# Performance work log

Measured on AMD Instinct MI355X. Metric: run time of the kernel, lower is better.

## Reference

```python
import jax, jax.numpy as jnp
import numpy as np

N_NODES = 50000
N_EDGES = 400000
H, D = 4, 32  # num_heads, per-head dim
NEG_SLOPE = 0.1


def setup_inputs() -> dict:
    key = jax.random.key(0)
    ks = jax.random.split(key, 12)
    inp = {
        'features': jax.random.normal(ks[0], (N_NODES, 256), jnp.float32) * 0.1,
        'src': jax.random.randint(ks[1], (N_EDGES,), 0, N_NODES, jnp.int32),
        'dst': jax.random.randint(ks[2], (N_EDGES,), 0, N_NODES, jnp.int32),
        'w': jax.random.uniform(ks[3], (N_EDGES,), jnp.float32),
        'W1': jax.random.normal(ks[4], (256, 128), jnp.float32) * 0.05,
        'al1': jax.random.normal(ks[5], (H, D), jnp.float32) * 0.1,
        'ar1': jax.random.normal(ks[6], (H, D), jnp.float32) * 0.1,
        'W2': jax.random.normal(ks[7], (128, 128), jnp.float32) * 0.05,
        'al2': jax.random.normal(ks[8], (H, D), jnp.float32) * 0.1,
        'ar2': jax.random.normal(ks[9], (H, D), jnp.float32) * 0.1,
        'Wout': jax.random.normal(ks[10], (256, 128), jnp.float32) * 0.05,
        'bout': jnp.zeros((128,), jnp.float32),
    }
    return inp


def _gat_layer(x, W, al, ar, src, dst, w):
    # x: [N, in_dim] -> ft: [N, H, D]
    ft = (x @ W).reshape(-1, H, D)
    el = jnp.einsum('nhd,hd->nh', ft, al)  # left attention logits per node
    er = jnp.einsum('nhd,hd->nh', ft, ar)
    # edge logits: leaky_relu(el[src] + er[dst]), then edge-weight scaling
    e = jax.nn.leaky_relu(el[src] + er[dst], negative_slope=NEG_SLOPE)  # [E, H]
    e = w[:, None] * e
    # segment softmax over incoming edges of each destination node
    m = jax.ops.segment_max(e, dst, num_segments=N_NODES)  # [N, H]
    a = jnp.exp(e - m[dst])
    s = jax.ops.segment_sum(a, dst, num_segments=N_NODES)
    a = a / s[dst]  # [E, H]
    # weighted scatter-sum aggregation: rst[dst] += a * ft[src]
    msg = ft[src] * a[:, :, None]  # [E, H, D]
    rst = jax.ops.segment_sum(msg, dst, num_segments=N_NODES)  # [N, H, D]
    # activation=relu, then concat heads (contiguous -> reshape)
    return jax.nn.relu(rst).reshape(-1, H * D)


def reference(features, src, dst, w, W1, al1, ar1, W2, al2, ar2, Wout, bout):
    x1 = _gat_layer(features, W1, al1, ar1, src, dst, w)  # [N, 128]
    x2 = _gat_layer(x1, W2, al2, ar2, src, dst, w)        # [N, 128]
    h = jnp.concatenate([x1, x2], axis=-1)                # [N, 256]
    return h @ Wout + bout                                # [N, 128]
```

## Files before the change

### kernel.cpp

```cpp
#include <hip/hip_runtime.h>
#include <math.h>

#define NEG_SLOPE 0.1f

typedef unsigned short u16;
typedef unsigned int u32;
typedef _Float16 f16;
typedef f16 f16x2 __attribute__((ext_vector_type(2)));
typedef f16 f16x8 __attribute__((ext_vector_type(8)));
typedef float f32x4 __attribute__((ext_vector_type(4)));

#define GLLDS16(g, l) __builtin_amdgcn_global_load_lds( \
    (const __attribute__((address_space(1))) void*)(g), \
    (__attribute__((address_space(3))) void*)(l), 16, 0, 0)


__device__ __forceinline__ void cast_panel(const float* __restrict__ W,
                                           const float* __restrict__ al,
                                           const float* __restrict__ ar,
                                           u16* __restrict__ bp, int t, int NC) {
    int per_kt = NC * 16;
    int kt = t / per_kt;
    int rem = t - kt * per_kt;
    int nt = rem >> 8;
    int w32 = rem & 255;
    int kg = w32 >> 6;
    int col = (w32 >> 2) & 15;
    int kp = (w32 & 3) * 2;
    int n = nt * 16 + col;
    int k = kt * 32 + kg * 8 + kp;
    float v0 = 0.f, v1 = 0.f;
    if (n < 128) {
        v0 = W[(size_t)k * 128 + n];
        v1 = W[(size_t)(k + 1) * 128 + n];
    } else if (n < 136) {
        const float* av = (n < 132) ? al : ar;
        int h = (n < 132) ? (n - 128) : (n - 132);
        float s0 = 0.f, s1 = 0.f;
        for (int d = 0; d < 32; d++) {
            float a = av[h * 32 + d];
            s0 += W[(size_t)k * 128 + h * 32 + d] * a;
            s1 += W[(size_t)(k + 1) * 128 + h * 32 + d] * a;
        }
        v0 = s0; v1 = s1;
    }
    f16x2 p;
    p.x = (f16)v0; p.y = (f16)v1;
    *(f16x2*)&((u32*)bp)[t] = p;
}

__global__ void histcast_k(const int* __restrict__ dst, int* __restrict__ cnt, int E,
                           const float* __restrict__ W1, const float* __restrict__ al1,
                           const float* __restrict__ ar1, u16* __restrict__ b1,
                           const float* __restrict__ W2, const float* __restrict__ al2,
                           const float* __restrict__ ar2, u16* __restrict__ b2,
                           const float* __restrict__ W3, u16* __restrict__ b3) {
    int t = blockIdx.x * 256 + threadIdx.x;
    if (t < E) atomicAdd(&cnt[dst[t]], 1);
    if (t < 18432) cast_panel(W1, al1, ar1, b1, t, 144);
    else if (t < 27648) cast_panel(W2, al2, ar2, b2, t - 18432, 144);
    else if (t < 44032) cast_panel(W3, nullptr, nullptr, b3, t - 27648, 128);
}


__global__ void assign_k(const int* __restrict__ cnt, int* __restrict__ start,
                         int* __restrict__ ctr, int N) {
    __shared__ int s[256];
    __shared__ int base;
    int t = threadIdx.x;
    int i = blockIdx.x * 256 + t;
    int v = (i < N) ? cnt[i] : 0;
    s[t] = v;
    __syncthreads();
    int incl = v;
    for (int off = 1; off < 256; off <<= 1) {
        int add = (t >= off) ? s[t - off] : 0;
        __syncthreads();
        incl += add;
        s[t] = incl;
        __syncthreads();
    }
    if (t == 255) base = atomicAdd(ctr, incl);
    __syncthreads();
    if (i < N) start[i] = base + incl - v;
}


template <int NT>
__device__ __forceinline__ void gemm_tile(
        const void* __restrict__ Av, int a_is_f16, int lda,
        const u16* __restrict__ Bp,
        const float* __restrict__ bias, float* __restrict__ Cf,
        u16* __restrict__ Ch, float* __restrict__ el, float* __restrict__ er,
        int M, int K, int tile, char* shmem) {
    u16* As = (u16*)shmem;
    u16* Bs = (u16*)(shmem + 8192);
    int tid = threadIdx.x;
    int wv = tid >> 6, lane = tid & 63;
    int mrow = lane & 15;
    int row0 = tile * 64;

    f32x4 acc[NT];
#pragma unroll
    for (int nt = 0; nt < NT; nt++) acc[nt] = (f32x4){0.f, 0.f, 0.f, 0.f};

    for (int k0 = 0; k0 < K; k0 += 64) {
        int kt0 = k0 >> 5;
        const u16* Bsrc = Bp + (size_t)kt0 * (NT * 512);
#pragma unroll
        for (int i = 0; i < (2 * NT * 64 + 255) / 256; i++) {
            int c = tid + i * 256;
            if (c < 2 * NT * 64) GLLDS16(Bsrc + (size_t)c * 8, &Bs[c * 8]);
        }
#pragma unroll
        for (int i = 0; i < 2; i++) {
            int c = tid + i * 256;
            int slice = c >> 8, w32 = c & 255;
            int rblk = w32 >> 6, kg = (w32 >> 4) & 3, rr = w32 & 15;
            int row = row0 + rblk * 16 + rr;
            int k = k0 + slice * 32 + kg * 8;
            if (a_is_f16) {
                const u16* Ah = (const u16*)Av;
                GLLDS16(Ah + (size_t)row * lda + k, &As[c * 8]);
            } else {
                const float* Af = (const float*)Av;
                if (row > M - 1) row = M - 1;
                const float* ap = &Af[(size_t)row * lda + k];
                float4 v0 = *(const float4*)ap;
                float4 v1 = *(const float4*)(ap + 4);
                f16x8 pk;
                pk[0] = (f16)v0.x; pk[1] = (f16)v0.y; pk[2] = (f16)v0.z; pk[3] = (f16)v0.w;
                pk[4] = (f16)v1.x; pk[5] = (f16)v1.y; pk[6] = (f16)v1.z; pk[7] = (f16)v1.w;
                *(f16x8*)&As[c * 8] = pk;
            }
        }
        __syncthreads();
#pragma unroll
        for (int kk = 0; kk < 2; kk++) {
            f16x8 ah = *(const f16x8*)&As[kk * 2048 + wv * 512 + lane * 8];
#pragma unroll
            for (int nt = 0; nt < NT; nt++) {
                f16x8 bh = *(const f16x8*)&Bs[kk * (NT * 512) + nt * 512 + lane * 8];
                acc[nt] = __builtin_amdgcn_mfma_f32_16x16x32_f16(ah, bh, acc[nt], 0, 0, 0);
            }
        }
        __syncthreads();
    }

    int rbase = row0 + wv * 16 + (lane >> 4) * 4;
#pragma unroll
    for (int nt = 0; nt < 8; nt++) {
        int col = nt * 16 + mrow;
        float bv = bias ? bias[col] : 0.f;
        f32x4 v = acc[nt];
#pragma unroll
        for (int reg = 0; reg < 4; reg++) {
            int rr = rbase + reg;
            if (rr < M) {
                float val = v[reg] + bv;
                if (Cf) Cf[(size_t)rr * 128 + col] = val;
                if (Ch) *(f16*)&Ch[(size_t)rr * 128 + col] = (f16)val;
            }
        }
    }
    if (NT == 9) {
        f32x4 v = acc[8];
#pragma unroll
        for (int reg = 0; reg < 4; reg++) {
            int rr = rbase + reg;
            if (rr < M) {
                if (mrow < 4) el[rr * 4 + mrow] = v[reg];
                else if (mrow < 8) er[rr * 4 + (mrow - 4)] = v[reg];
            }
        }
    }
}

template <int NT>
__global__ __launch_bounds__(256) void gemm_k(
        const void* __restrict__ Av, int a_is_f16, int lda,
        const u16* __restrict__ Bp, const float* __restrict__ bias,
        float* __restrict__ Cf, u16* __restrict__ Ch,
        float* __restrict__ el, float* __restrict__ er, int M, int K) {
    alignas(16) __shared__ char sh[8192 + NT * 2048];
    gemm_tile<NT>(Av, a_is_f16, lda, Bp, bias, Cf, Ch, el, er, M, K, blockIdx.x, sh);
}

__global__ __launch_bounds__(256) void g1s_k(
        const float* __restrict__ features, const u16* __restrict__ b1,
        u16* __restrict__ fth, float* __restrict__ el, float* __restrict__ er,
        int M, int gb,
        const int* __restrict__ src, const int* __restrict__ dst,
        const float* __restrict__ w, const int* __restrict__ start,
        int* __restrict__ fill, int2* __restrict__ edge_s, int E) {
    alignas(16) __shared__ char sh[8192 + 9 * 2048];
    if ((int)blockIdx.x < gb) {
        gemm_tile<9>(features, 0, 256, b1, nullptr, nullptr, fth, el, er,
                     M, 256, blockIdx.x, sh);
    } else {
        int e = (blockIdx.x - gb) * 256 + threadIdx.x;
        if (e < E) {
            int d = dst[e];
            int pos = atomicAdd(&fill[d], 1);
            edge_s[start[d] + pos] = make_int2(src[e], __float_as_int(w[e]));
        }
    }
}


__device__ __forceinline__ float lrelu(float x) {
    return x > 0.f ? x : NEG_SLOPE * x;
}

__global__ __launch_bounds__(256) void agg_k(const u32* __restrict__ fth2,
                                             const float4* __restrict__ el4,
                                             const float4* __restrict__ er4,
                                             const int2* __restrict__ edge_s,
                                             const int* __restrict__ start,
                                             const int* __restrict__ cnt,
                                             u16* __restrict__ xcat,
                                             int ooff, int N, int ngroups) {
    __shared__ float4 sA[256];
    __shared__ int sS[256];
    int wv = threadIdx.x >> 6;
    int lane = threadIdx.x & 63;
    int head = lane >> 4;
    for (int g = blockIdx.x; g < ngroups; g += gridDim.x) {
        int n = g * 4 + wv;
        if (n >= N) continue;
        int r0 = start[n], deg = cnt[n];
        u16* op = &xcat[(size_t)n * 256 + ooff + 2 * lane];
        if (deg == 0) {
            *(u32*)op = 0;
            continue;
        }
        float4 ern = er4[n];
        float acc0 = 0.f, acc1 = 0.f;
        if (deg <= 64) {
            float4 a = make_float4(0.f, 0.f, 0.f, 0.f);
            int s = 0;
            if (lane < deg) {
                int2 ep = edge_s[r0 + lane];
                s = ep.x;
                float we = __int_as_float(ep.y);
                float4 e = el4[s];
                a.x = __expf(we * lrelu(e.x + ern.x));
                a.y = __expf(we * lrelu(e.y + ern.y));
                a.z = __expf(we * lrelu(e.z + ern.z));
                a.w = __expf(we * lrelu(e.w + ern.w));
            }
            float4 sm = a;
            for (int m = 1; m < deg; m <<= 1) {
                sm.x += __shfl_xor(sm.x, m);
                sm.y += __shfl_xor(sm.y, m);
                sm.z += __shfl_xor(sm.z, m);
                sm.w += __shfl_xor(sm.w, m);
            }
            a.x *= __builtin_amdgcn_rcpf(sm.x);
            a.y *= __builtin_amdgcn_rcpf(sm.y);
            a.z *= __builtin_amdgcn_rcpf(sm.z);
            a.w *= __builtin_amdgcn_rcpf(sm.w);
            sA[wv * 64 + lane] = a;
            sS[wv * 64 + lane] = s;
            const float* sAf = (const float*)&sA[wv * 64];
            const int* sSp = &sS[wv * 64];
            int i = 0;
            for (; i + 8 <= deg; i += 8) {
                float wg[8];
                u32 pp[8];
#pragma unroll
                for (int j = 0; j < 8; j++) {
                    wg[j] = sAf[(i + j) * 4 + head];
                    pp[j] = fth2[(size_t)sSp[i + j] * 64 + lane];
                }
#pragma unroll
                for (int j = 0; j < 8; j++) {
                    f16x2 hp = *(const f16x2*)&pp[j];
                    acc0 += wg[j] * (float)hp.x;
                    acc1 += wg[j] * (float)hp.y;
                }
            }
            for (; i < deg; i++) {
                float wgt = sAf[i * 4 + head];
                u32 p = fth2[(size_t)sSp[i] * 64 + lane];
                f16x2 hp = *(const f16x2*)&p;
                acc0 += wgt * (float)hp.x;
                acc1 += wgt * (float)hp.y;
            }
        } else {
            float4 mx = make_float4(-INFINITY, -INFINITY, -INFINITY, -INFINITY);
            for (int i = lane; i < deg; i += 64) {
                int2 ep = edge_s[r0 + i];
                float we = __int_as_float(ep.y);
                float4 e = el4[ep.x];
                mx.x = fmaxf(mx.x, we * lrelu(e.x + ern.x));
                mx.y = fmaxf(mx.y, we * lrelu(e.y + ern.y));
                mx.z = fmaxf(mx.z, we * lrelu(e.z + ern.z));
                mx.w = fmaxf(mx.w, we * lrelu(e.w + ern.w));
            }
            for (int m = 32; m >= 1; m >>= 1) {
                mx.x = fmaxf(mx.x, __shfl_xor(mx.x, m));
                mx.y = fmaxf(mx.y, __shfl_xor(mx.y, m));
                mx.z = fmaxf(mx.z, __shfl_xor(mx.z, m));
                mx.w = fmaxf(mx.w, __shfl_xor(mx.w, m));
            }
            float4 sm = make_float4(0.f, 0.f, 0.f, 0.f);
            for (int i = lane; i < deg; i += 64) {
                int2 ep = edge_s[r0 + i];
                float we = __int_as_float(ep.y);
                float4 e = el4[ep.x];
                sm.x += __expf(we * lrelu(e.x + ern.x) - mx.x);
                sm.y += __expf(we * lrelu(e.y + ern.y) - mx.y);
                sm.z += __expf(we * lrelu(e.z + ern.z) - mx.z);
                sm.w += __expf(we * lrelu(e.w + ern.w) - mx.w);
            }
            for (int m = 32; m >= 1; m >>= 1) {
                sm.x += __shfl_xor(sm.x, m);
                sm.y += __shfl_xor(sm.y, m);
                sm.z += __shfl_xor(sm.z, m);
                sm.w += __shfl_xor(sm.w, m);
            }
            float4 inv;
            inv.x = 1.f / sm.x; inv.y = 1.f / sm.y;
            inv.z = 1.f / sm.z; inv.w = 1.f / sm.w;
            for (int i = 0; i < deg; i++) {
                int2 ep = edge_s[r0 + i];
                int si = ep.x;
                float we = __int_as_float(ep.y);
                float4 e = el4[si];
                float ax = __expf(we * lrelu(e.x + ern.x) - mx.x) * inv.x;
                float ay = __expf(we * lrelu(e.y + ern.y) - mx.y) * inv.y;
                float az = __expf(we * lrelu(e.z + ern.z) - mx.z) * inv.z;
                float aw = __expf(we * lrelu(e.w + ern.w) - mx.w) * inv.w;
                float wgt = head == 0 ? ax : (head == 1 ? ay : (head == 2 ? az : aw));
                u32 p = fth2[(size_t)si * 64 + lane];
                f16x2 hp = *(const f16x2*)&p;
                acc0 += wgt * (float)hp.x;
                acc1 += wgt * (float)hp.y;
            }
        }
        f16x2 hv;
        hv.x = (f16)fmaxf(acc0, 0.f);
        hv.y = (f16)fmaxf(acc1, 0.f);
        *(f16x2*)op = hv;
    }
}


extern "C" void kernel_launch(void* const* d_in, const int* in_sizes, int n_in,
                              void* d_out, int out_size, void* d_ws, size_t ws_size,
                              hipStream_t stream) {
    const float* features = (const float*)d_in[0];
    const int* src = (const int*)d_in[1];
    const int* dst = (const int*)d_in[2];
    const float* w = (const float*)d_in[3];
    const float* W1 = (const float*)d_in[4];
    const float* al1 = (const float*)d_in[5];
    const float* ar1 = (const float*)d_in[6];
    const float* W2 = (const float*)d_in[7];
    const float* al2 = (const float*)d_in[8];
    const float* ar2 = (const float*)d_in[9];
    const float* Wout = (const float*)d_in[10];
    const float* bout = (const float*)d_in[11];
    float* out = (float*)d_out;

    int N = in_sizes[0] / 256;
    int E = in_sizes[1];
    int Mpad = ((N + 127) / 128) * 128;

    char* ws = (char*)d_ws;
    size_t off = 0;
    auto alloc = [&](size_t bytes) -> void* {
        void* p = ws + off;
        off = (off + bytes + 255) & ~(size_t)255;
        return p;
    };
    size_t Nr = ((size_t)N * 4 + 255) & ~(size_t)255;
    int* cnt = (int*)alloc(2 * Nr + 256);
    int* fill = (int*)((char*)cnt + Nr);
    int* ctr = (int*)((char*)cnt + 2 * Nr);
    int* start = (int*)alloc((size_t)N * 4);
    int2* edge_s = (int2*)alloc((size_t)E * 8);
    u16* fth = (u16*)alloc((size_t)Mpad * 128 * 2);
    float* el = (float*)alloc((size_t)N * 4 * 4);
    float* er = (float*)alloc((size_t)N * 4 * 4);
    u16* xcat = (u16*)alloc((size_t)Mpad * 256 * 2);
    u16* b1 = (u16*)alloc((size_t)18432 * 4);
    u16* b2 = (u16*)alloc((size_t)9216 * 4);
    u16* b3 = (u16*)alloc((size_t)16384 * 4);
    (void)ws_size; (void)n_in; (void)out_size;

    (void)hipMemsetAsync(cnt, 0, 2 * Nr + 256, stream);

    int eb = (E + 255) / 256;
    int nb = (N + 255) / 256;
    int ng = (N + 3) / 4;
    int ab = ng < 2048 ? ng : 2048;
    int gb = Mpad / 64;

    histcast_k<<<eb, 256, 0, stream>>>(dst, cnt, E, W1, al1, ar1, b1,
                                       W2, al2, ar2, b2, Wout, b3);
    assign_k<<<nb, 256, 0, stream>>>(cnt, start, ctr, N);

    g1s_k<<<gb + eb, 256, 0, stream>>>(features, b1, fth, el, er, N, gb,
                                       src, dst, w, start, fill, edge_s, E);
    agg_k<<<ab, 256, 0, stream>>>((const u32*)fth, (const float4*)el, (const float4*)er,
                                  edge_s, start, cnt, xcat, 0, N, ng);

    gemm_k<9><<<gb, 256, 0, stream>>>(xcat, 1, 256, b2, nullptr,
                                      nullptr, fth, el, er, N, 128);
    agg_k<<<ab, 256, 0, stream>>>((const u32*)fth, (const float4*)el, (const float4*)er,
                                  edge_s, start, cnt, xcat, 128, N, ng);

    gemm_k<8><<<gb, 256, 0, stream>>>(xcat, 1, 256, b3, bout,
                                      out, nullptr, nullptr, nullptr, N, 256);
}
```

Before: 247.6 us.

## Fuse neighbor aggregation with following GEMM into single aggemm kernel

Replaces separate agg_k and gemm_k launches with a fused aggemm_k kernel. Each block aggregates 64 destination rows directly into the LDS A-tile in MFMA layout, then runs the GEMM from shared memory. Layer-1 output is still written to global memory for reuse as half of the final concat input. Feature buffers are double-buffered to avoid read/write hazards. This removes two launches and the global round trip of aggregated features. The cost is less parallelism: only gb blocks each do 16 sequential nodes per wave, where the old agg kernel used up to 2048 blocks with a grid-stride loop.

New measurement: 329.4 us. 33.0% more time.

```diff
diff --git a/kernel.cpp b/kernel.cpp
--- a/kernel.cpp
+++ b/kernel.cpp
@@ -176,16 +176,6 @@
     }
 }
 
-template <int NT>
-__global__ __launch_bounds__(256) void gemm_k(
-        const void* __restrict__ Av, int a_is_f16, int lda,
-        const u16* __restrict__ Bp, const float* __restrict__ bias,
-        float* __restrict__ Cf, u16* __restrict__ Ch,
-        float* __restrict__ el, float* __restrict__ er, int M, int K) {
-    alignas(16) __shared__ char sh[8192 + NT * 2048];
-    gemm_tile<NT>(Av, a_is_f16, lda, Bp, bias, Cf, Ch, el, er, M, K, blockIdx.x, sh);
-}
-
 __global__ __launch_bounds__(256) void g1s_k(
         const float* __restrict__ features, const u16* __restrict__ b1,
         u16* __restrict__ fth, float* __restrict__ el, float* __restrict__ er,
@@ -212,137 +202,229 @@
     return x > 0.f ? x : NEG_SLOPE * x;
 }
 
-__global__ __launch_bounds__(256) void agg_k(const u32* __restrict__ fth2,
-                                             const float4* __restrict__ el4,
-                                             const float4* __restrict__ er4,
-                                             const int2* __restrict__ edge_s,
-                                             const int* __restrict__ start,
-                                             const int* __restrict__ cnt,
-                                             u16* __restrict__ xcat,
-                                             int ooff, int N, int ngroups) {
-    __shared__ float4 sA[256];
+__device__ __forceinline__ u32 agg_node(const u32* __restrict__ fth2,
+                                        const float4* __restrict__ el4,
+                                        const float4* __restrict__ er4,
+                                        const int2* __restrict__ edge_s,
+                                        const int* __restrict__ start,
+                                        const int* __restrict__ cnt,
+                                        int n, int lane, int head,
+                                        float4* sAw, int* sSw) {
+    int r0 = start[n], deg = cnt[n];
+    if (deg == 0) return 0u;
+    float4 ern = er4[n];
+    float acc0 = 0.f, acc1 = 0.f;
+    if (deg <= 64) {
+        float4 a = make_float4(0.f, 0.f, 0.f, 0.f);
+        int s = 0;
+        if (lane < deg) {
+            int2 ep = edge_s[r0 + lane];
+            s = ep.x;
+            float we = __int_as_float(ep.y);
+            float4 e = el4[s];
+            a.x = __expf(we * lrelu(e.x + ern.x));
+            a.y = __expf(we * lrelu(e.y + ern.y));
+            a.z = __expf(we * lrelu(e.z + ern.z));
+            a.w = __expf(we * lrelu(e.w + ern.w));
+        }
+        float4 sm = a;
+        for (int m = 1; m < deg; m <<= 1) {
+            sm.x += __shfl_xor(sm.x, m);
+            sm.y += __shfl_xor(sm.y, m);
+            sm.z += __shfl_xor(sm.z, m);
+            sm.w += __shfl_xor(sm.w, m);
+        }
+        a.x *= __builtin_amdgcn_rcpf(sm.x);
+        a.y *= __builtin_amdgcn_rcpf(sm.y);
+        a.z *= __builtin_amdgcn_rcpf(sm.z);
+        a.w *= __builtin_amdgcn_rcpf(sm.w);
+        sAw[lane] = a;
+        sSw[lane] = s;
+        const float* sAf = (const float*)sAw;
+        int i = 0;
+        for (; i + 8 <= deg; i += 8) {
+            float wg[8];
+            u32 pp[8];
+#pragma unroll
+            for (int j = 0; j < 8; j++) {
+                wg[j] = sAf[(i + j) * 4 + head];
+                pp[j] = fth2[(size_t)sSw[i + j] * 64 + lane];
+            }
+#pragma unroll
+            for (int j = 0; j < 8; j++) {
+                f16x2 hp = *(const f16x2*)&pp[j];
+                acc0 += wg[j] * (float)hp.x;
+                acc1 += wg[j] * (float)hp.y;
+            }
+        }
+        for (; i < deg; i++) {
+            float wgt = sAf[i * 4 + head];
+            u32 p = fth2[(size_t)sSw[i] * 64 + lane];
+            f16x2 hp = *(const f16x2*)&p;
+            acc0 += wgt * (float)hp.x;
+            acc1 += wgt * (float)hp.y;
+        }
+    } else {
+        float4 mx = make_float4(-INFINITY, -INFINITY, -INFINITY, -INFINITY);
+        for (int i = lane; i < deg; i += 64) {
+            int2 ep = edge_s[r0 + i];
+            float we = __int_as_float(ep.y);
+            float4 e = el4[ep.x];
+            mx.x = fmaxf(mx.x, we * lrelu(e.x + ern.x));
+            mx.y = fmaxf(mx.y, we * lrelu(e.y + ern.y));
+            mx.z = fmaxf(mx.z, we * lrelu(e.z + ern.z));
+            mx.w = fmaxf(mx.w, we * lrelu(e.w + ern.w));
+        }
+        for (int m = 32; m >= 1; m >>= 1) {
+            mx.x = fmaxf(mx.x, __shfl_xor(mx.x, m));
+            mx.y = fmaxf(mx.y, __shfl_xor(mx.y, m));
+            mx.z = fmaxf(mx.z, __shfl_xor(mx.z, m));
+            mx.w = fmaxf(mx.w, __shfl_xor(mx.w, m));
+        }
+        float4 sm = make_float4(0.f, 0.f, 0.f, 0.f);
+        for (int i = lane; i < deg; i += 64) {
+            int2 ep = edge_s[r0 + i];
+            float we = __int_as_float(ep.y);
+            float4 e = el4[ep.x];
+            sm.x += __expf(we * lrelu(e.x + ern.x) - mx.x);
+            sm.y += __expf(we * lrelu(e.y + ern.y) - mx.y);
+            sm.z += __expf(we * lrelu(e.z + ern.z) - mx.z);
+            sm.w += __expf(we * lrelu(e.w + ern.w) - mx.w);
+        }
+        for (int m = 32; m >= 1; m >>= 1) {
+            sm.x += __shfl_xor(sm.x, m);
+            sm.y += __shfl_xor(sm.y, m);
+            sm.z += __shfl_xor(sm.z, m);
+            sm.w += __shfl_xor(sm.w, m);
+        }
+        float4 inv;
+        inv.x = 1.f / sm.x; inv.y = 1.f / sm.y;
+        inv.z = 1.f / sm.z; inv.w = 1.f / sm.w;
+        for (int i = 0; i < deg; i++) {
+            int2 ep = edge_s[r0 + i];
+            int si = ep.x;
+            float we = __int_as_float(ep.y);
+            float4 e = el4[si];
+            float ax = __expf(we * lrelu(e.x + ern.x) - mx.x) * inv.x;
+            float ay = __expf(we * lrelu(e.y + ern.y) - mx.y) * inv.y;
+            float az = __expf(we * lrelu(e.z + ern.z) - mx.z) * inv.z;
+            float aw = __expf(we * lrelu(e.w + ern.w) - mx.w) * inv.w;
+            float wgt = head == 0 ? ax : (head == 1 ? ay : (head == 2 ? az : aw));
+            u32 p = fth2[(size_t)si * 64 + lane];
+            f16x2 hp = *(const f16x2*)&p;
+            acc0 += wgt * (float)hp.x;
+            acc1 += wgt * (float)hp.y;
+        }
+    }
+    f16x2 hv;
+    hv.x = (f16)fmaxf(acc0, 0.f);
+    hv.y = (f16)fmaxf(acc1, 0.f);
+    u32 b;
+    __builtin_memcpy(&b, &hv, 4);
+    return b;
+}
+
+
+template <int NT, int KS, int SL0>
+__global__ __launch_bounds__(256) void aggemm_k(
+        const u32* __restrict__ fth_in, const float4* __restrict__ el_in,
+        const float4* __restrict__ er_in, const int2* __restrict__ edge_s,
+        const int* __restrict__ start, const int* __restrict__ cnt,
+        const u16* __restrict__ x1g, const u16* __restrict__ Bp,
+        const float* __restrict__ bias, float* __restrict__ Cf,
+        u16* __restrict__ Ch, float* __restrict__ el_out,
+        float* __restrict__ er_out, u16* __restrict__ x1out, int N) {
+    alignas(16) __shared__ u16 As[KS * 2 * 2048];
+    alignas(16) __shared__ u16 Bs[2 * NT * 512];
+    alignas(16) __shared__ float4 sA[256];
     __shared__ int sS[256];
-    int wv = threadIdx.x >> 6;
-    int lane = threadIdx.x & 63;
+    int tid = threadIdx.x, wv = tid >> 6, lane = tid & 63;
+    int mrow = lane & 15;
+    int row0 = blockIdx.x * 64;
+
+#pragma unroll
+    for (int i = 0; i < (2 * NT * 64 + 255) / 256; i++) {
+        int c = tid + i * 256;
+        if (c < 2 * NT * 64) GLLDS16(Bp + (size_t)c * 8, &Bs[c * 8]);
+    }
+    if (SL0 == 4) {
+#pragma unroll
+        for (int i = 0; i < 4; i++) {
+            int c = tid + i * 256;
+            int slice = c >> 8, w32 = c & 255;
+            int rblk = w32 >> 6, kg = (w32 >> 4) & 3, rr = w32 & 15;
+            int row = row0 + rblk * 16 + rr;
+            GLLDS16(x1g + (size_t)row * 128 + slice * 32 + kg * 8, &As[c * 8]);
+        }
+    }
     int head = lane >> 4;
-    for (int g = blockIdx.x; g < ngroups; g += gridDim.x) {
-        int n = g * 4 + wv;
-        if (n >= N) continue;
-        int r0 = start[n], deg = cnt[n];
-        u16* op = &xcat[(size_t)n * 256 + ooff + 2 * lane];
-        if (deg == 0) {
-            *(u32*)op = 0;
-            continue;
-        }
-        float4 ern = er4[n];
-        float acc0 = 0.f, acc1 = 0.f;
-        if (deg <= 64) {
-            float4 a = make_float4(0.f, 0.f, 0.f, 0.f);
-            int s = 0;
-            if (lane < deg) {
-                int2 ep = edge_s[r0 + lane];
-                s = ep.x;
-                float we = __int_as_float(ep.y);
-                float4 e = el4[s];
-                a.x = __expf(we * lrelu(e.x + ern.x));
-                a.y = __expf(we * lrelu(e.y + ern.y));
-                a.z = __expf(we * lrelu(e.z + ern.z));
-                a.w = __expf(we * lrelu(e.w + ern.w));
-            }
-            float4 sm = a;
-            for (int m = 1; m < deg; m <<= 1) {
-                sm.x += __shfl_xor(sm.x, m);
-                sm.y += __shfl_xor(sm.y, m);
-                sm.z += __shfl_xor(sm.z, m);
-                sm.w += __shfl_xor(sm.w, m);
-            }
-            a.x *= __builtin_amdgcn_rcpf(sm.x);
-            a.y *= __builtin_amdgcn_rcpf(sm.y);
-            a.z *= __builtin_amdgcn_rcpf(sm.z);
-            a.w *= __builtin_amdgcn_rcpf(sm.w);
-            sA[wv * 64 + lane] = a;
-            sS[wv * 64 + lane] = s;
-            const float* sAf = (const float*)&sA[wv * 64];
-            const int* sSp = &sS[wv * 64];
-            int i = 0;
-            for (; i + 8 <= deg; i += 8) {
-                float wg[8];
-                u32 pp[8];
-#pragma unroll
-                for (int j = 0; j < 8; j++) {
-                    wg[j] = sAf[(i + j) * 4 + head];
-                    pp[j] = fth2[(size_t)sSp[i + j] * 64 + lane];
-                }
-#pragma unroll
-                for (int j = 0; j < 8; j++) {
-                    f16x2 hp = *(const f16x2*)&pp[j];
-                    acc0 += wg[j] * (float)hp.x;
-                    acc1 += wg[j] * (float)hp.y;
-                }
-            }
-            for (; i < deg; i++) {
-                float wgt = sAf[i * 4 + head];
-                u32 p = fth2[(size_t)sSp[i] * 64 + lane];
-                f16x2 hp = *(const f16x2*)&p;
-                acc0 += wgt * (float)hp.x;
-                acc1 += wgt * (float)hp.y;
-            }
-        } else {
-            float4 mx = make_float4(-INFINITY, -INFINITY, -INFINITY, -INFINITY);
-            for (int i = lane; i < deg; i += 64) {
-                int2 ep = edge_s[r0 + i];
-                float we = __int_as_float(ep.y);
-                float4 e = el4[ep.x];
-                mx.x = fmaxf(mx.x, we * lrelu(e.x + ern.x));
-                mx.y = fmaxf(mx.y, we * lrelu(e.y + ern.y));
-                mx.z = fmaxf(mx.z, we * lrelu(e.z + ern.z));
-                mx.w = fmaxf(mx.w, we * lrelu(e.w + ern.w));
-            }
-            for (int m = 32; m >= 1; m >>= 1) {
-                mx.x = fmaxf(mx.x, __shfl_xor(mx.x, m));
-                mx.y = fmaxf(mx.y, __shfl_xor(mx.y, m));
-                mx.z = fmaxf(mx.z, __shfl_xor(mx.z, m));
-                mx.w = fmaxf(mx.w, __shfl_xor(mx.w, m));
-            }
-            float4 sm = make_float4(0.f, 0.f, 0.f, 0.f);
-            for (int i = lane; i < deg; i += 64) {
-                int2 ep = edge_s[r0 + i];
-                float we = __int_as_float(ep.y);
-                float4 e = el4[ep.x];
-                sm.x += __expf(we * lrelu(e.x + ern.x) - mx.x);
-                sm.y += __expf(we * lrelu(e.y + ern.y) - mx.y);
-                sm.z += __expf(we * lrelu(e.z + ern.z) - mx.z);
-                sm.w += __expf(we * lrelu(e.w + ern.w) - mx.w);
-            }
-            for (int m = 32; m >= 1; m >>= 1) {
-                sm.x += __shfl_xor(sm.x, m);
-                sm.y += __shfl_xor(sm.y, m);
-                sm.z += __shfl_xor(sm.z, m);
-                sm.w += __shfl_xor(sm.w, m);
-            }
-            float4 inv;
-            inv.x = 1.f / sm.x; inv.y = 1.f / sm.y;
-            inv.z = 1.f / sm.z; inv.w = 1.f / sm.w;
-            for (int i = 0; i < deg; i++) {
-                int2 ep = edge_s[r0 + i];
-                int si = ep.x;
-                float we = __int_as_float(ep.y);
-                float4 e = el4[si];
-                float ax = __expf(we * lrelu(e.x + ern.x) - mx.x) * inv.x;
-                float ay = __expf(we * lrelu(e.y + ern.y) - mx.y) * inv.y;
-                float az = __expf(we * lrelu(e.z + ern.z) - mx.z) * inv.z;
-                float aw = __expf(we * lrelu(e.w + ern.w) - mx.w) * inv.w;
-                float wgt = head == 0 ? ax : (head == 1 ? ay : (head == 2 ? az : aw));
-                u32 p = fth2[(size_t)si * 64 + lane];
-                f16x2 hp = *(const f16x2*)&p;
-                acc0 += wgt * (float)hp.x;
-                acc1 += wgt * (float)hp.y;
-            }
-        }
-        f16x2 hv;
-        hv.x = (f16)fmaxf(acc0, 0.f);
-        hv.y = (f16)fmaxf(acc1, 0.f);
-        *(f16x2*)op = hv;
+    for (int j = 0; j < 16; j++) {
+        int r = (wv << 4) + j;
+        int n = row0 + r;
+        u32 hv = (n < N) ? agg_node(fth_in, el_in, er_in, edge_s, start, cnt,
+                                    n, lane, head, &sA[wv * 64], &sS[wv * 64])
+                         : 0u;
+        int d0 = lane * 2;
+        int off = (((d0 >> 5) + SL0) * 256 + ((r >> 4) << 6) +
+                   (((d0 >> 3) & 3) << 4) + (r & 15)) * 8 + (d0 & 7);
+        *(u32*)&As[off] = hv;
+        if (x1out && n < N) *(u32*)&x1out[(size_t)n * 128 + d0] = hv;
+    }
+    __syncthreads();
+
+    f32x4 acc[NT];
+#pragma unroll
+    for (int nt = 0; nt < NT; nt++) acc[nt] = (f32x4){0.f, 0.f, 0.f, 0.f};
+#pragma unroll
+    for (int ks = 0; ks < KS; ks++) {
+        if (ks) {
+            __syncthreads();
+#pragma unroll
+            for (int i = 0; i < (2 * NT * 64 + 255) / 256; i++) {
+                int c = tid + i * 256;
+                if (c < 2 * NT * 64)
+                    GLLDS16(Bp + (size_t)(2 * ks) * (NT * 512) + (size_t)c * 8,
+                            &Bs[c * 8]);
+            }
+            __syncthreads();
+        }
+#pragma unroll
+        for (int kk = 0; kk < 2; kk++) {
+            f16x8 ah = *(const f16x8*)&As[(ks * 2 + kk) * 2048 + wv * 512 + lane * 8];
+#pragma unroll
+            for (int nt = 0; nt < NT; nt++) {
+                f16x8 bh = *(const f16x8*)&Bs[kk * (NT * 512) + nt * 512 + lane * 8];
+                acc[nt] = __builtin_amdgcn_mfma_f32_16x16x32_f16(ah, bh, acc[nt], 0, 0, 0);
+            }
+        }
+    }
+
+    int rbase = row0 + wv * 16 + (lane >> 4) * 4;
+#pragma unroll
+    for (int nt = 0; nt < 8; nt++) {
+        int col = nt * 16 + mrow;
+        float bv = bias ? bias[col] : 0.f;
+        f32x4 v = acc[nt];
+#pragma unroll
+        for (int reg = 0; reg < 4; reg++) {
+            int rr = rbase + reg;
+            if (rr < N) {
+                float val = v[reg] + bv;
+                if (Cf) Cf[(size_t)rr * 128 + col] = val;
+                if (Ch) *(f16*)&Ch[(size_t)rr * 128 + col] = (f16)val;
+            }
+        }
+    }
+    if (NT == 9) {
+        f32x4 v = acc[8];
+#pragma unroll
+        for (int reg = 0; reg < 4; reg++) {
+            int rr = rbase + reg;
+            if (rr < N) {
+                if (mrow < 4) el_out[rr * 4 + mrow] = v[reg];
+                else if (mrow < 8) er_out[rr * 4 + (mrow - 4)] = v[reg];
+            }
+        }
     }
 }
 
@@ -381,10 +463,13 @@
     int* ctr = (int*)((char*)cnt + 2 * Nr);
     int* start = (int*)alloc((size_t)N * 4);
     int2* edge_s = (int2*)alloc((size_t)E * 8);
-    u16* fth = (u16*)alloc((size_t)Mpad * 128 * 2);
-    float* el = (float*)alloc((size_t)N * 4 * 4);
-    float* er = (float*)alloc((size_t)N * 4 * 4);
-    u16* xcat = (u16*)alloc((size_t)Mpad * 256 * 2);
+    u16* fthA = (u16*)alloc((size_t)Mpad * 128 * 2);
+    u16* fthB = (u16*)alloc((size_t)Mpad * 128 * 2);
+    float* elA = (float*)alloc((size_t)N * 4 * 4);
+    float* erA = (float*)alloc((size_t)N * 4 * 4);
+    float* elB = (float*)alloc((size_t)N * 4 * 4);
+    float* erB = (float*)alloc((size_t)N * 4 * 4);
+    u16* xcat = (u16*)alloc((size_t)Mpad * 128 * 2);
     u16* b1 = (u16*)alloc((size_t)18432 * 4);
     u16* b2 = (u16*)alloc((size_t)9216 * 4);
     u16* b3 = (u16*)alloc((size_t)16384 * 4);
@@ -394,24 +479,22 @@
 
     int eb = (E + 255) / 256;
     int nb = (N + 255) / 256;
-    int ng = (N + 3) / 4;
-    int ab = ng < 2048 ? ng : 2048;
     int gb = Mpad / 64;
 
     histcast_k<<<eb, 256, 0, stream>>>(dst, cnt, E, W1, al1, ar1, b1,
                                        W2, al2, ar2, b2, Wout, b3);
     assign_k<<<nb, 256, 0, stream>>>(cnt, start, ctr, N);
 
-    g1s_k<<<gb + eb, 256, 0, stream>>>(features, b1, fth, el, er, N, gb,
+    g1s_k<<<gb + eb, 256, 0, stream>>>(features, b1, fthA, elA, erA, N, gb,
                                        src, dst, w, start, fill, edge_s, E);
-    agg_k<<<ab, 256, 0, stream>>>((const u32*)fth, (const float4*)el, (const float4*)er,
-                                  edge_s, start, cnt, xcat, 0, N, ng);
-
-    gemm_k<9><<<gb, 256, 0, stream>>>(xcat, 1, 256, b2, nullptr,
-                                      nullptr, fth, el, er, N, 128);
-    agg_k<<<ab, 256, 0, stream>>>((const u32*)fth, (const float4*)el, (const float4*)er,
-                                  edge_s, start, cnt, xcat, 128, N, ng);
-
-    gemm_k<8><<<gb, 256, 0, stream>>>(xcat, 1, 256, b3, bout,
-                                      out, nullptr, nullptr, nullptr, N, 256);
-}
+
+    aggemm_k<9, 2, 0><<<gb, 256, 0, stream>>>(
+        (const u32*)fthA, (const float4*)elA, (const float4*)erA,
+        edge_s, start, cnt, nullptr, b2, nullptr,
+        nullptr, fthB, elB, erB, xcat, N);
+
+    aggemm_k<8, 4, 4><<<gb, 256, 0, stream>>>(
+        (const u32*)fthB, (const float4*)elB, (const float4*)erB,
+        edge_s, start, cnt, xcat, b3, bout,
+        out, nullptr, nullptr, nullptr, nullptr, N);
+}
```
